# Optimization experiments

Measured on AMD Instinct MI355X. Metric: run time of the kernel, lower is better.

## Reference

```python
import jax, jax.numpy as jnp
import numpy as np
import math

WINDOW_SIZE = 11
SIGMA = 1.5
CHANNELS = 3
C1 = 0.01 ** 2
C2 = 0.03 ** 2
PAD = WINDOW_SIZE // 2


def make_window():
    # 1D gaussian, normalized, then outer product -> (C, 1, K, K) depthwise kernel
    xs = np.arange(WINDOW_SIZE)
    g = np.exp(-((xs - WINDOW_SIZE // 2) ** 2) / (2.0 * SIGMA ** 2))
    g = (g / g.sum()).astype(np.float32)
    w2d = np.outer(g, g)  # (K, K)
    w = np.broadcast_to(w2d[None, None], (CHANNELS, 1, WINDOW_SIZE, WINDOW_SIZE))
    return jnp.asarray(np.ascontiguousarray(w))


def _dwconv(x, window):
    # depthwise conv2d, groups = channels, 'same' padding for odd K
    return jax.lax.conv_general_dilated(
        x, window,
        window_strides=(1, 1),
        padding=[(PAD, PAD), (PAD, PAD)],
        dimension_numbers=("NCHW", "OIHW", "NCHW"),
        feature_group_count=CHANNELS,
    )


def _ssim_loss(img1, img2, window):
    mu1 = _dwconv(img1, window)
    mu2 = _dwconv(img2, window)
    mu1_sq = mu1 * mu1
    mu2_sq = mu2 * mu2
    mu1_mu2 = mu1 * mu2
    sigma1_sq = _dwconv(img1 * img1, window) - mu1_sq
    sigma2_sq = _dwconv(img2 * img2, window) - mu2_sq
    sigma12 = _dwconv(img1 * img2, window) - mu1_mu2
    ssim_map = ((2.0 * mu1_mu2 + C1) * (2.0 * sigma12 + C2)) / (
        (mu1_sq + mu2_sq + C1) * (sigma1_sq + sigma2_sq + C2)
    )
    return 1.0 - jnp.mean(ssim_map)  # reduction='mean'


def setup_inputs() -> dict:
    key = jax.random.key(0)
    k1, k2 = jax.random.split(key)
    B, C, H, W = 4, 3, 1088, 1920
    img1 = jax.random.uniform(k1, (B, C, H, W), dtype=jnp.float32)
    img2 = jax.random.uniform(k2, (B, C, H, W), dtype=jnp.float32)
    window = make_window()
    return {"img1": img1, "img2": img2, "window": window}


def reference(img1, img2, window):
    return _ssim_loss(img1, img2, window)
```

## Files before the change

### kernel.cpp

```cpp
#include <hip/hip_runtime.h>


namespace {
constexpr int IW   = 1920;
constexpr int IH   = 1088;
constexpr int NPL  = 12;
constexpr int TW   = 128;
constexpr int TH   = 64;
constexpr int HALO = 5;
constexpr int RW   = TW + 2 * HALO;
constexpr int RWP  = 140;
constexpr int TX   = IW / TW;
constexpr int TY   = IH / TH;
constexpr int NTILE = TX * TY * NPL;
constexpr int NSTEP = TH + 2 * HALO;
constexpr float C1v = 0.0001f;
constexpr float C2v = 0.0009f;
constexpr double NPIX = 25067520.0;

__device__ constexpr float WT[11] = {
    0.00102838f, 0.00759876f, 0.03600077f, 0.10936062f, 0.21300553f,
    0.26601172f,
    0.21300553f, 0.10936062f, 0.03600077f, 0.00759876f, 0.00102838f};
}

__device__ __forceinline__ float ssim_px(const float v[5]) {
    float mu1 = v[0], mu2 = v[1];
    float mu1s = mu1 * mu1, mu2s = mu2 * mu2, mu12 = mu1 * mu2;
    float s1 = v[2] - mu1s;
    float s2 = v[3] - mu2s;
    float s12 = v[4] - mu12;
    float num = (2.0f * mu12 + C1v) * (2.0f * s12 + C2v);
    float den = (mu1s + mu2s + C1v) * (s1 + s2 + C2v);
    return num * __builtin_amdgcn_rcpf(den);
}

__global__ __launch_bounds__(256) void ssim_main(const float* __restrict__ img1,
                                                 const float* __restrict__ img2,
                                                 double* __restrict__ acc) {
    const int lane = threadIdx.x & 63;
    const int wv   = threadIdx.x >> 6;
    const int wid  = blockIdx.x * 4 + wv;

    const int tx  = wid % TX;
    const int t2  = wid / TX;
    const int ty  = t2 % TY;
    const int pl  = t2 / TY;
    const int X0  = tx * TW - HALO;
    const int Y0  = ty * TH - HALO;

    const float* __restrict__ base1 = img1 + (long long)pl * IH * IW;
    const float* __restrict__ base2 = img2 + (long long)pl * IH * IW;

    __shared__ float lds[4][2][RWP];
    float* __restrict__ l1 = lds[wv][0];
    float* __restrict__ l2 = lds[wv][1];

    float win0[5][11], win1[5][11];
    float r1[3], r2[3];
    float sum = 0.0f;

    auto loadrow = [&](int r, float v1[3], float v2[3]) {
        const int gy = Y0 + r;
        const bool gok = (gy >= 0) && (gy < IH);
        const long long roff = (long long)gy * IW;
#pragma unroll
        for (int k = 0; k < 3; ++k) {
            const int pos = lane + 64 * k;
            float a = 0.0f, b = 0.0f;
            if (gok && pos < RW) {
                const int gx = X0 + pos;
                if (gx >= 0 && gx < IW) {
                    a = base1[roff + gx];
                    b = base2[roff + gx];
                }
            }
            v1[k] = a;
            v2[k] = b;
        }
    };

    loadrow(0, r1, r2);

    for (int rb = 0; rb < NSTEP; rb += 11) {
#pragma unroll
        for (int jj = 0; jj < 11; ++jj) {
            const int r = rb + jj;
            if (r < NSTEP) {
#pragma unroll
                for (int k = 0; k < 3; ++k) {
                    const int pos = lane + 64 * k;
                    if (pos < RW) {
                        l1[pos] = r1[k];
                        l2[pos] = r2[k];
                    }
                }
                if (r + 1 < NSTEP) loadrow(r + 1, r1, r2);

                float a[12], b[12];
#pragma unroll
                for (int i = 0; i < 6; ++i) {
                    const float2 ta = *(const float2*)(l1 + 2 * lane + 2 * i);
                    const float2 tb = *(const float2*)(l2 + 2 * lane + 2 * i);
                    a[2 * i] = ta.x; a[2 * i + 1] = ta.y;
                    b[2 * i] = tb.x; b[2 * i + 1] = tb.y;
                }

                float h0[5] = {0, 0, 0, 0, 0};
                float h1[5] = {0, 0, 0, 0, 0};
#pragma unroll
                for (int i = 0; i < 12; ++i) {
                    const float ai = a[i], bi = b[i];
                    const float pr[5] = {ai, bi, ai * ai, bi * bi, ai * bi};
                    if (i < 11) {
#pragma unroll
                        for (int q = 0; q < 5; ++q) h0[q] += WT[i] * pr[q];
                    }
                    if (i > 0) {
#pragma unroll
                        for (int q = 0; q < 5; ++q) h1[q] += WT[i - 1] * pr[q];
                    }
                }
#pragma unroll
                for (int q = 0; q < 5; ++q) {
                    win0[q][jj] = h0[q];
                    win1[q][jj] = h1[q];
                }

                if (r >= 10) {
                    float v0[5] = {0, 0, 0, 0, 0};
                    float v1v[5] = {0, 0, 0, 0, 0};
#pragma unroll
                    for (int m = 0; m < 11; ++m) {
                        const int s = (jj + 1 + m) % 11;
                        const float w = WT[m];
#pragma unroll
                        for (int q = 0; q < 5; ++q) {
                            v0[q]  += w * win0[q][s];
                            v1v[q] += w * win1[q][s];
                        }
                    }
                    sum += ssim_px(v0) + ssim_px(v1v);
                }
            }
        }
    }

#pragma unroll
    for (int off = 32; off > 0; off >>= 1) sum += __shfl_down(sum, off);
    if (lane == 0) atomicAdd(acc, (double)sum);
}

__global__ void ssim_fin(const double* __restrict__ acc, float* __restrict__ out) {
    if (threadIdx.x == 0) out[0] = 1.0f - (float)(acc[0] / NPIX);
}

extern "C" void kernel_launch(void* const* d_in, const int* in_sizes, int n_in,
                              void* d_out, int out_size, void* d_ws, size_t ws_size,
                              hipStream_t stream) {
    const float* img1 = (const float*)d_in[0];
    const float* img2 = (const float*)d_in[1];
    float* out = (float*)d_out;
    double* acc = (double*)d_ws;

    hipMemsetAsync(acc, 0, sizeof(double), stream);
    ssim_main<<<dim3(NTILE / 4), dim3(256), 0, stream>>>(img1, img2, acc);
    ssim_fin<<<1, 64, 0, stream>>>(acc, out);
}
```

Measured before the change: 308.3 us.

## Compute separable Gaussian convolutions with fp16 MFMA banded-matrix products

Replaces the scalar FMA horizontal and vertical 11-tap filters with 16x16x32 fp16 MFMA operations against banded Gaussian weight matrices. The five moment fields are staged in a swizzled fp16 LDS ring. Tiles shrink to 32x64 and global loads become vectorised float4 on interior tiles. The aim is to move the FLOP-heavy convolution work onto matrix cores, at the cost of fp16 precision for the inputs, squares and intermediate sums. The variance terms are computed as differences of these values and may lose accuracy through cancellation.

```diff
diff --git a/kernel.cpp b/kernel.cpp
--- a/kernel.cpp
+++ b/kernel.cpp
@@ -1,150 +1,164 @@
 #include <hip/hip_runtime.h>
 
 
+typedef _Float16 half8  __attribute__((ext_vector_type(8)));
+typedef float    f32x4  __attribute__((ext_vector_type(4)));
+
 namespace {
-constexpr int IW   = 1920;
-constexpr int IH   = 1088;
-constexpr int NPL  = 12;
-constexpr int TW   = 128;
-constexpr int TH   = 64;
-constexpr int HALO = 5;
-constexpr int RW   = TW + 2 * HALO;
-constexpr int RWP  = 140;
-constexpr int TX   = IW / TW;
-constexpr int TY   = IH / TH;
+constexpr int IW  = 1920;
+constexpr int IH  = 1088;
+constexpr int NPL = 12;
+constexpr int TW  = 32;
+constexpr int TH  = 64;
+constexpr int TX  = IW / TW;
+constexpr int TY  = IH / TH;
 constexpr int NTILE = TX * TY * NPL;
-constexpr int NSTEP = TH + 2 * HALO;
 constexpr float C1v = 0.0001f;
 constexpr float C2v = 0.0009f;
 constexpr double NPIX = 25067520.0;
-
-__device__ constexpr float WT[11] = {
-    0.00102838f, 0.00759876f, 0.03600077f, 0.10936062f, 0.21300553f,
-    0.26601172f,
-    0.21300553f, 0.10936062f, 0.03600077f, 0.00759876f, 0.00102838f};
 }
 
-__device__ __forceinline__ float ssim_px(const float v[5]) {
-    float mu1 = v[0], mu2 = v[1];
-    float mu1s = mu1 * mu1, mu2s = mu2 * mu2, mu12 = mu1 * mu2;
-    float s1 = v[2] - mu1s;
-    float s2 = v[3] - mu2s;
-    float s12 = v[4] - mu12;
-    float num = (2.0f * mu12 + C1v) * (2.0f * s12 + C2v);
-    float den = (mu1s + mu2s + C1v) * (s1 + s2 + C2v);
-    return num * __builtin_amdgcn_rcpf(den);
-}
-
-__global__ __launch_bounds__(256) void ssim_main(const float* __restrict__ img1,
-                                                 const float* __restrict__ img2,
-                                                 double* __restrict__ acc) {
+__global__ __launch_bounds__(256, 4) void ssim_main(const float* __restrict__ img1,
+                                                    const float* __restrict__ img2,
+                                                    double* __restrict__ acc) {
     const int lane = threadIdx.x & 63;
     const int wv   = threadIdx.x >> 6;
     const int wid  = blockIdx.x * 4 + wv;
 
-    const int tx  = wid % TX;
-    const int t2  = wid / TX;
-    const int ty  = t2 % TY;
-    const int pl  = t2 / TY;
-    const int X0  = tx * TW - HALO;
-    const int Y0  = ty * TH - HALO;
+    const int tx = wid % TX;
+    const int t2 = wid / TX;
+    const int ty = t2 % TY;
+    const int pl = t2 / TY;
+
+    const int l15 = lane & 15;
+    const int lg  = lane >> 4;
+
+    const int X0 = tx * TW;
+    const int Y0 = ty * TH - 5;
 
     const float* __restrict__ base1 = img1 + (long long)pl * IH * IW;
     const float* __restrict__ base2 = img2 + (long long)pl * IH * IW;
 
-    __shared__ float lds[4][2][RWP];
-    float* __restrict__ l1 = lds[wv][0];
-    float* __restrict__ l2 = lds[wv][1];
+    half8 wH, wV;
+#pragma unroll
+    for (int i = 0; i < 8; ++i) {
+        const int k   = lg * 8 + i;
+        const int iv  = k - l15;
+        const int ih2 = iv - 3;
+        const int dv = iv - 5, dh = ih2 - 5;
+        const float ev = __expf((float)(dv * dv) * (-1.0f / 4.5f)) * 0.26601172f;
+        const float eh = __expf((float)(dh * dh) * (-1.0f / 4.5f)) * 0.26601172f;
+        wV[i] = (_Float16)((iv  >= 0 && iv  <= 10) ? ev : 0.0f);
+        wH[i] = (_Float16)((ih2 >= 0 && ih2 <= 10) ? eh : 0.0f);
+    }
 
-    float win0[5][11], win1[5][11];
-    float r1[3], r2[3];
+    __shared__ _Float16 ringall[4][5][32][32];
+    _Float16* __restrict__ rg = &ringall[wv][0][0][0];
+
     float sum = 0.0f;
+    const f32x4 zz = {0.0f, 0.0f, 0.0f, 0.0f};
 
-    auto loadrow = [&](int r, float v1[3], float v2[3]) {
-        const int gy = Y0 + r;
-        const bool gok = (gy >= 0) && (gy < IH);
-        const long long roff = (long long)gy * IW;
+    auto store4 = [](_Float16* p, f32x4 c) {
+        const unsigned int lo =
+            __builtin_bit_cast(unsigned int, __builtin_amdgcn_cvt_pkrtz(c[0], c[1]));
+        const unsigned int hi =
+            __builtin_bit_cast(unsigned int, __builtin_amdgcn_cvt_pkrtz(c[2], c[3]));
+        uint2 u; u.x = lo; u.y = hi;
+        *(uint2*)p = u;
+    };
+
+    auto hgroup = [&](int g) {
+        const int gy = Y0 + 16 * g + l15;
+        const bool rowok = ((unsigned)gy < (unsigned)IH);
+        const long long rbase = (long long)gy * IW;
+        const bool safe = (tx > 0) && (tx < TX - 1) &&
+                          !(ty == 0 && g == 0) && !(ty == TY - 1 && g == 4);
 #pragma unroll
-        for (int k = 0; k < 3; ++k) {
-            const int pos = lane + 64 * k;
-            float a = 0.0f, b = 0.0f;
-            if (gok && pos < RW) {
-                const int gx = X0 + pos;
-                if (gx >= 0 && gx < IW) {
-                    a = base1[roff + gx];
-                    b = base2[roff + gx];
+        for (int ct = 0; ct < 2; ++ct) {
+            const int gx0 = X0 - 8 + 16 * ct + lg * 8;
+            float av[8], bv[8];
+            if (safe) {
+                const float4* pa = (const float4*)(base1 + rbase + gx0);
+                const float4* pb = (const float4*)(base2 + rbase + gx0);
+                const float4 a0 = pa[0], a1 = pa[1];
+                const float4 b0 = pb[0], b1 = pb[1];
+                av[0] = a0.x; av[1] = a0.y; av[2] = a0.z; av[3] = a0.w;
+                av[4] = a1.x; av[5] = a1.y; av[6] = a1.z; av[7] = a1.w;
+                bv[0] = b0.x; bv[1] = b0.y; bv[2] = b0.z; bv[3] = b0.w;
+                bv[4] = b1.x; bv[5] = b1.y; bv[6] = b1.z; bv[7] = b1.w;
+            } else {
+#pragma unroll
+                for (int e = 0; e < 8; ++e) {
+                    const int gx = gx0 + e;
+                    const bool ok = rowok && (gx >= 0) && (gx < IW);
+                    av[e] = ok ? base1[rbase + gx] : 0.0f;
+                    bv[e] = ok ? base2[rbase + gx] : 0.0f;
                 }
             }
-            v1[k] = a;
-            v2[k] = b;
+            half8 af, bf;
+#pragma unroll
+            for (int e = 0; e < 8; ++e) {
+                af[e] = (_Float16)av[e];
+                bf[e] = (_Float16)bv[e];
+            }
+            const half8 aa = af * af;
+            const half8 bb = bf * bf;
+            const half8 ab = af * bf;
+
+            const f32x4 c0 = __builtin_amdgcn_mfma_f32_16x16x32_f16(af, wH, zz, 0, 0, 0);
+            const f32x4 c1 = __builtin_amdgcn_mfma_f32_16x16x32_f16(bf, wH, zz, 0, 0, 0);
+            const f32x4 c2 = __builtin_amdgcn_mfma_f32_16x16x32_f16(aa, wH, zz, 0, 0, 0);
+            const f32x4 c3 = __builtin_amdgcn_mfma_f32_16x16x32_f16(bb, wH, zz, 0, 0, 0);
+            const f32x4 c4 = __builtin_amdgcn_mfma_f32_16x16x32_f16(ab, wH, zz, 0, 0, 0);
+
+            const int col = 16 * ct + l15;
+            const int rs  = (16 * g + lg * 4) & 31;
+            const int rbs = (rs >> 3) ^ (col & 3);
+            _Float16* wp = rg + col * 32 + rbs * 8 + (rs & 7);
+            store4(wp + 0 * 1024, c0);
+            store4(wp + 1 * 1024, c1);
+            store4(wp + 2 * 1024, c2);
+            store4(wp + 3 * 1024, c3);
+            store4(wp + 4 * 1024, c4);
         }
     };
 
-    loadrow(0, r1, r2);
+    auto vtile = [&](int t) {
+#pragma unroll
+        for (int vc = 0; vc < 2; ++vc) {
+            const int col = 16 * vc + l15;
+            const int rs0 = (16 * t + lg * 8) & 31;
+            const int rbs = (rs0 >> 3) ^ (col & 3);
+            const _Float16* rp = rg + col * 32 + rbs * 8;
 
-    for (int rb = 0; rb < NSTEP; rb += 11) {
+            const f32x4 a0 = __builtin_amdgcn_mfma_f32_16x16x32_f16(wV, *(const half8*)(rp + 0 * 1024), zz, 0, 0, 0);
+            const f32x4 a1 = __builtin_amdgcn_mfma_f32_16x16x32_f16(wV, *(const half8*)(rp + 1 * 1024), zz, 0, 0, 0);
+            const f32x4 a2 = __builtin_amdgcn_mfma_f32_16x16x32_f16(wV, *(const half8*)(rp + 2 * 1024), zz, 0, 0, 0);
+            const f32x4 a3 = __builtin_amdgcn_mfma_f32_16x16x32_f16(wV, *(const half8*)(rp + 3 * 1024), zz, 0, 0, 0);
+            const f32x4 a4 = __builtin_amdgcn_mfma_f32_16x16x32_f16(wV, *(const half8*)(rp + 4 * 1024), zz, 0, 0, 0);
+
 #pragma unroll
-        for (int jj = 0; jj < 11; ++jj) {
-            const int r = rb + jj;
-            if (r < NSTEP) {
-#pragma unroll
-                for (int k = 0; k < 3; ++k) {
-                    const int pos = lane + 64 * k;
-                    if (pos < RW) {
-                        l1[pos] = r1[k];
-                        l2[pos] = r2[k];
-                    }
-                }
-                if (r + 1 < NSTEP) loadrow(r + 1, r1, r2);
-
-                float a[12], b[12];
-#pragma unroll
-                for (int i = 0; i < 6; ++i) {
-                    const float2 ta = *(const float2*)(l1 + 2 * lane + 2 * i);
-                    const float2 tb = *(const float2*)(l2 + 2 * lane + 2 * i);
-                    a[2 * i] = ta.x; a[2 * i + 1] = ta.y;
-                    b[2 * i] = tb.x; b[2 * i + 1] = tb.y;
-                }
-
-                float h0[5] = {0, 0, 0, 0, 0};
-                float h1[5] = {0, 0, 0, 0, 0};
-#pragma unroll
-                for (int i = 0; i < 12; ++i) {
-                    const float ai = a[i], bi = b[i];
-                    const float pr[5] = {ai, bi, ai * ai, bi * bi, ai * bi};
-                    if (i < 11) {
-#pragma unroll
-                        for (int q = 0; q < 5; ++q) h0[q] += WT[i] * pr[q];
-                    }
-                    if (i > 0) {
-#pragma unroll
-                        for (int q = 0; q < 5; ++q) h1[q] += WT[i - 1] * pr[q];
-                    }
-                }
-#pragma unroll
-                for (int q = 0; q < 5; ++q) {
-                    win0[q][jj] = h0[q];
-                    win1[q][jj] = h1[q];
-                }
-
-                if (r >= 10) {
-                    float v0[5] = {0, 0, 0, 0, 0};
-                    float v1v[5] = {0, 0, 0, 0, 0};
-#pragma unroll
-                    for (int m = 0; m < 11; ++m) {
-                        const int s = (jj + 1 + m) % 11;
-                        const float w = WT[m];
-#pragma unroll
-                        for (int q = 0; q < 5; ++q) {
-                            v0[q]  += w * win0[q][s];
-                            v1v[q] += w * win1[q][s];
-                        }
-                    }
-                    sum += ssim_px(v0) + ssim_px(v1v);
-                }
+            for (int i = 0; i < 4; ++i) {
+                const float mu1 = a0[i], mu2 = a1[i];
+                const float ea = a2[i], eb = a3[i], eab = a4[i];
+                const float mu1s = mu1 * mu1, mu2s = mu2 * mu2, mu12 = mu1 * mu2;
+                const float s1 = ea - mu1s, s2 = eb - mu2s, s12 = eab - mu12;
+                const float num = (2.0f * mu12 + C1v) * (2.0f * s12 + C2v);
+                const float den = (mu1s + mu2s + C1v) * (s1 + s2 + C2v);
+                sum += num * __builtin_amdgcn_rcpf(den);
             }
         }
-    }
+    };
+
+    hgroup(0);
+    hgroup(1);
+    vtile(0);
+    hgroup(2);
+    vtile(1);
+    hgroup(3);
+    vtile(2);
+    hgroup(4);
+    vtile(3);
 
 #pragma unroll
     for (int off = 32; off > 0; off >>= 1) sum += __shfl_down(sum, off);
@@ -158,12 +172,13 @@
 extern "C" void kernel_launch(void* const* d_in, const int* in_sizes, int n_in,
                               void* d_out, int out_size, void* d_ws, size_t ws_size,
                               hipStream_t stream) {
+    (void)in_sizes; (void)n_in; (void)out_size; (void)ws_size;
     const float* img1 = (const float*)d_in[0];
     const float* img2 = (const float*)d_in[1];
     float* out = (float*)d_out;
     double* acc = (double*)d_ws;
 
-    hipMemsetAsync(acc, 0, sizeof(double), stream);
+    (void)hipMemsetAsync(acc, 0, sizeof(double), stream);
     ssim_main<<<dim3(NTILE / 4), dim3(256), 0, stream>>>(img1, img2, acc);
     ssim_fin<<<1, 64, 0, stream>>>(acc, out);
 }
```

Measured after the change: 344.1 us. 1.12x slower.
